# Kernel tuning notes

Hardware: AMD Instinct MI355X
Metric: run time of the kernel (lower is better)

Reference implementation:

```python
import jax, jax.numpy as jnp
import numpy as np

N_NODES = 100000
N_REL = 2
N_EDGES = 1600000  # per relation, avg degree 16
F_IN = 128
F_OUT = 64


def setup_inputs() -> dict:
    key = jax.random.key(0)
    k1, k2, k3, k4, k5 = jax.random.split(key, 5)
    x = jax.random.normal(k1, (N_NODES, F_IN), dtype=jnp.float32)
    src = jax.random.randint(k2, (N_REL, N_EDGES), 0, N_NODES)
    dst = jax.random.randint(k3, (N_REL, N_EDGES), 0, N_NODES)
    edge_w = jax.random.uniform(k4, (N_REL, N_EDGES), dtype=jnp.float32)
    # xavier_uniform with gain=1.414 as in the torch module
    limit = 1.414 * np.sqrt(6.0 / (F_IN + F_OUT))
    W = jax.random.uniform(k5, (F_IN, F_OUT), dtype=jnp.float32,
                           minval=-limit, maxval=limit)
    return {"x": x, "W": W, "edge_w": edge_w, "src": src, "dst": dst}


def reference(x, W, edge_w, src, dst):
    # Original: for each relation r, h = X @ W; support_r = A_r @ h; out = relu(sum_r support_r)
    # Since h is identical across relations and results are summed, compute
    # X @ W once and aggregate all relations' edges in one fused scatter-add.
    n = x.shape[0]
    h = x @ W  # [N, F_OUT]
    s = src.reshape(-1)  # [R*E]
    d = dst.reshape(-1)  # [R*E]
    w = edge_w.reshape(-1, 1)  # [R*E, 1]
    msgs = w * h[s]  # [R*E, F_OUT] weighted gather of source features
    agg = jax.ops.segment_sum(msgs, d, num_segments=n)  # [N, F_OUT]
    return jax.nn.relu(agg)
```

## Files before the change

### kernel.cpp

```cpp
#include <hip/hip_runtime.h>
#include <hip/hip_bf16.h>
#include <stdint.h>

#define F_IN 128
#define F_OUT 64
#define NPB 128
#define CHUNK 4096
#define NBUCK_MAX 1024
#define SRC_BITS 17
#define BCAP 5120

static __device__ __forceinline__ unsigned short f2bf(float f) {
    uint32_t u = __float_as_uint(f);
    u += 0x7FFF + ((u >> 16) & 1);
    return (unsigned short)(u >> 16);
}
static __device__ __forceinline__ float bf2f(unsigned short s) {
    return __uint_as_float((uint32_t)s << 16);
}

extern "C" __global__ __launch_bounds__(256) void k1_fused(
        const float* __restrict__ x, const float* __restrict__ W,
        unsigned short* __restrict__ h, int n,
        const int* __restrict__ src, const int* __restrict__ dst,
        const float* __restrict__ ew, int* __restrict__ cursor,
        uint32_t* __restrict__ rec32, uint8_t* __restrict__ dlo8,
        long nE, int nbuck, int partBlocks) {
    extern __shared__ char smem[];
    const int tid = threadIdx.x;

    if ((int)blockIdx.x < partBlocks) {
        uint32_t* srec  = (uint32_t*)smem;
        int*      cnt   = (int*)(smem + CHUNK * 4);
        int*      lbase = cnt + NBUCK_MAX;
        int*      gbase = lbase + NBUCK_MAX;
        int*      ssc   = gbase + NBUCK_MAX;
        uint8_t*  sdlo  = (uint8_t*)(ssc + 256);

        const int  c      = blockIdx.x;
        const long base   = (long)c * CHUNK;
        const long endl   = base + CHUNK < nE ? base + CHUNK : nE;
        const int  tcount = (int)(endl - base);

        for (int i = tid; i < NBUCK_MAX; i += 256) cnt[i] = 0;
        __syncthreads();
        for (int i = tid; i < tcount; i += 256)
            atomicAdd(&cnt[dst[base + i] >> 7], 1);
        __syncthreads();
        {
            const int t4 = tid * 4;
            const int a0 = cnt[t4], a1 = cnt[t4 + 1], a2 = cnt[t4 + 2], a3 = cnt[t4 + 3];
            const int ts = a0 + a1 + a2 + a3;
            ssc[tid] = ts; __syncthreads();
            for (int o = 1; o < 256; o <<= 1) {
                int t = (tid >= o) ? ssc[tid - o] : 0;
                __syncthreads();
                ssc[tid] += t;
                __syncthreads();
            }
            const int e = ssc[tid] - ts;
            lbase[t4]     = e;
            lbase[t4 + 1] = e + a0;
            lbase[t4 + 2] = e + a0 + a1;
            lbase[t4 + 3] = e + a0 + a1 + a2;
        }
        __syncthreads();
        for (int k = tid; k < nbuck; k += 256) {
            const int ck = cnt[k];
            if (ck) gbase[k] = k * BCAP + atomicAdd(&cursor[k], ck);
        }
        __syncthreads();
        for (int i = tid; i < NBUCK_MAX; i += 256) cnt[i] = lbase[i];
        __syncthreads();
        for (int i = tid; i < tcount; i += 256) {
            const int d = dst[base + i];
            const int k = d >> 7;
            const int pos = atomicAdd(&cnt[k], 1);
            uint32_t u = __float_as_uint(ew[base + i]);
            u += 0x10000u;
            srec[pos] = (u & 0xFFFE0000u) | (uint32_t)src[base + i];
            sdlo[pos] = (uint8_t)(d & (NPB - 1));
        }
        __syncthreads();
        for (int j = tid; j < tcount; j += 256) {
            int k = 0;
#pragma unroll
            for (int s = 512; s > 0; s >>= 1) {
                const int nk = k + s;
                if (nk < NBUCK_MAX && lbase[nk] <= j) k = nk;
            }
            const int gpos = gbase[k] + (j - lbase[k]);
            rec32[gpos] = srec[j];
            dlo8[gpos]  = sdlo[j];
        }
        return;
    }

    float* Ws = (float*)smem;
    float (*Xs)[F_IN + 4] = (float(*)[F_IN + 4])(smem + F_IN * F_OUT * 4);
    const int gb = (int)blockIdx.x - partBlocks;
    for (int i = tid; i < F_IN * F_OUT / 4; i += 256)
        ((float4*)Ws)[i] = ((const float4*)W)[i];
    const int row0 = gb * 16;
    for (int i = tid; i < 16 * 32; i += 256) {
        int r = i >> 5, cc = i & 31;
        if (row0 + r < n)
            *(float4*)&Xs[r][cc * 4] = *(const float4*)(x + (size_t)(row0 + r) * F_IN + cc * 4);
    }
    __syncthreads();
    const int cg = tid & 15;
    const int r  = tid >> 4;
    const int row = row0 + r;
    float4 acc = make_float4(0.f, 0.f, 0.f, 0.f);
#pragma unroll
    for (int k = 0; k < F_IN; ++k) {
        float  xv = Xs[r][k];
        float4 wv = ((const float4*)Ws)[k * 16 + cg];
        acc.x = fmaf(xv, wv.x, acc.x);
        acc.y = fmaf(xv, wv.y, acc.y);
        acc.z = fmaf(xv, wv.z, acc.z);
        acc.w = fmaf(xv, wv.w, acc.w);
    }
    if (row < n) {
        ushort4 o;
        o.x = f2bf(acc.x); o.y = f2bf(acc.y); o.z = f2bf(acc.z); o.w = f2bf(acc.w);
        *(ushort4*)(h + (size_t)row * F_OUT + cg * 4) = o;
    }
}

__global__ __launch_bounds__(256) void sortB(uint32_t* __restrict__ rec,
                                             const uint8_t* __restrict__ dlo8,
                                             const int* __restrict__ cursor,
                                             int* __restrict__ obeg,
                                             int* __restrict__ oend,
                                             int n, int nbuck) {
    __shared__ uint32_t ssort[BCAP];
    __shared__ int cnt[NPB], run[NPB], sa[NPB], sb[NPB];
    const int k   = blockIdx.x;
    const int tid = threadIdx.x;
    const int rbase = k * BCAP;
    int m = cursor[k];
    if (m > BCAP) m = BCAP;
    if (tid < NPB) cnt[tid] = 0;
    __syncthreads();
    for (int i = tid; i < m; i += 256)
        atomicAdd(&cnt[dlo8[(long)rbase + i]], 1);
    __syncthreads();
    if (tid < NPB) sa[tid] = cnt[tid];
    __syncthreads();
    int* pin = sa; int* pout = sb;
    for (int o = 1; o < NPB; o <<= 1) {
        if (tid < NPB) pout[tid] = pin[tid] + (tid >= o ? pin[tid - o] : 0);
        __syncthreads();
        int* t = pin; pin = pout; pout = t;
    }
    if (tid < NPB) {
        const int e = pin[tid] - cnt[tid];
        run[tid] = e;
        const int node = k * NPB + tid;
        if (node < n) {
            obeg[node] = rbase + e;
            oend[node] = rbase + e + cnt[tid];
        }
    }
    __syncthreads();
    for (int i = tid; i < m; i += 256) {
        const uint32_t r = rec[(long)rbase + i];
        const int d = dlo8[(long)rbase + i];
        ssort[atomicAdd(&run[d], 1)] = r;
    }
    __syncthreads();
    for (int i = tid; i < m; i += 256)
        rec[(long)rbase + i] = ssort[i];
}

__global__ __launch_bounds__(256, 8) void gather_nodes(
        const unsigned short* __restrict__ h,
        const uint32_t* __restrict__ rec,
        const int* __restrict__ obeg,
        const int* __restrict__ oend,
        float* __restrict__ out, int n) {
    const int wid  = threadIdx.x >> 6;
    const int lane = threadIdx.x & 63;
    const int node = blockIdx.x * 4 + wid;
    if (node >= n) return;
    int j = obeg[node];
    const int end = oend[node];
    const uint32_t M = (1u << SRC_BITS) - 1;
    float acc = 0.f;
    for (; j < end && (j & 3); ++j) {
        const uint32_t s = rec[j];
        acc = fmaf(__uint_as_float(s & 0xFFFE0000u),
                   bf2f(h[(int)((s & M) * 64u) + lane]), acc);
    }
    for (; j + 8 <= end; j += 8) {
        const uint4 A = *(const uint4*)(rec + j);
        const uint4 B = *(const uint4*)(rec + j + 4);
        const int i0 = (int)((A.x & M) * 64u) + lane;
        const int i1 = (int)((A.y & M) * 64u) + lane;
        const int i2 = (int)((A.z & M) * 64u) + lane;
        const int i3 = (int)((A.w & M) * 64u) + lane;
        const int i4 = (int)((B.x & M) * 64u) + lane;
        const int i5 = (int)((B.y & M) * 64u) + lane;
        const int i6 = (int)((B.z & M) * 64u) + lane;
        const int i7 = (int)((B.w & M) * 64u) + lane;
        const unsigned short d0 = h[i0];
        const unsigned short d1 = h[i1];
        const unsigned short d2 = h[i2];
        const unsigned short d3 = h[i3];
        const unsigned short d4 = h[i4];
        const unsigned short d5 = h[i5];
        const unsigned short d6 = h[i6];
        const unsigned short d7 = h[i7];
        acc = fmaf(__uint_as_float(A.x & 0xFFFE0000u), bf2f(d0), acc);
        acc = fmaf(__uint_as_float(A.y & 0xFFFE0000u), bf2f(d1), acc);
        acc = fmaf(__uint_as_float(A.z & 0xFFFE0000u), bf2f(d2), acc);
        acc = fmaf(__uint_as_float(A.w & 0xFFFE0000u), bf2f(d3), acc);
        acc = fmaf(__uint_as_float(B.x & 0xFFFE0000u), bf2f(d4), acc);
        acc = fmaf(__uint_as_float(B.y & 0xFFFE0000u), bf2f(d5), acc);
        acc = fmaf(__uint_as_float(B.z & 0xFFFE0000u), bf2f(d6), acc);
        acc = fmaf(__uint_as_float(B.w & 0xFFFE0000u), bf2f(d7), acc);
    }
    if (j + 4 <= end) {
        const uint4 A = *(const uint4*)(rec + j);
        const int i0 = (int)((A.x & M) * 64u) + lane;
        const int i1 = (int)((A.y & M) * 64u) + lane;
        const int i2 = (int)((A.z & M) * 64u) + lane;
        const int i3 = (int)((A.w & M) * 64u) + lane;
        const unsigned short d0 = h[i0];
        const unsigned short d1 = h[i1];
        const unsigned short d2 = h[i2];
        const unsigned short d3 = h[i3];
        acc = fmaf(__uint_as_float(A.x & 0xFFFE0000u), bf2f(d0), acc);
        acc = fmaf(__uint_as_float(A.y & 0xFFFE0000u), bf2f(d1), acc);
        acc = fmaf(__uint_as_float(A.z & 0xFFFE0000u), bf2f(d2), acc);
        acc = fmaf(__uint_as_float(A.w & 0xFFFE0000u), bf2f(d3), acc);
        j += 4;
    }
    for (; j < end; ++j) {
        const uint32_t s = rec[j];
        acc = fmaf(__uint_as_float(s & 0xFFFE0000u),
                   bf2f(h[(int)((s & M) * 64u) + lane]), acc);
    }
    out[(size_t)node * F_OUT + lane] = fmaxf(acc, 0.f);
}

__global__ __launch_bounds__(256) void gemm_only(const float* __restrict__ x,
                                                 const float* __restrict__ W,
                                                 unsigned short* __restrict__ h, int n) {
    __shared__ float Ws[F_IN * F_OUT];
    __shared__ float Xs[16][F_IN + 4];
    for (int i = threadIdx.x; i < F_IN * F_OUT / 4; i += 256)
        ((float4*)Ws)[i] = ((const float4*)W)[i];
    const int row0 = blockIdx.x * 16;
    for (int i = threadIdx.x; i < 16 * 32; i += 256) {
        int r = i >> 5, c = i & 31;
        if (row0 + r < n)
            *(float4*)&Xs[r][c * 4] = *(const float4*)(x + (size_t)(row0 + r) * F_IN + c * 4);
    }
    __syncthreads();
    const int cg = threadIdx.x & 15;
    const int r  = threadIdx.x >> 4;
    const int row = row0 + r;
    float4 acc = make_float4(0.f, 0.f, 0.f, 0.f);
#pragma unroll
    for (int k = 0; k < F_IN; ++k) {
        float  xv = Xs[r][k];
        float4 wv = ((const float4*)Ws)[k * 16 + cg];
        acc.x = fmaf(xv, wv.x, acc.x);
        acc.y = fmaf(xv, wv.y, acc.y);
        acc.z = fmaf(xv, wv.z, acc.z);
        acc.w = fmaf(xv, wv.w, acc.w);
    }
    if (row < n) {
        ushort4 o;
        o.x = f2bf(acc.x); o.y = f2bf(acc.y); o.z = f2bf(acc.z); o.w = f2bf(acc.w);
        *(ushort4*)(h + (size_t)row * F_OUT + cg * 4) = o;
    }
}

__global__ __launch_bounds__(256) void scatter_edges(const unsigned short* __restrict__ h,
                                                     const float* __restrict__ edge_w,
                                                     const int* __restrict__ src,
                                                     const int* __restrict__ dst,
                                                     float* __restrict__ out, long n_edges) {
    const int lane = threadIdx.x & 63;
    const long wave = ((long)blockIdx.x * blockDim.x + threadIdx.x) >> 6;
    const long nwaves = ((long)gridDim.x * blockDim.x) >> 6;
    for (long e = wave; e < n_edges; e += nwaves) {
        const float v = edge_w[e] * bf2f(h[(size_t)src[e] * F_OUT + lane]);
        atomicAdd(&out[(size_t)dst[e] * F_OUT + lane], v);
    }
}

__global__ __launch_bounds__(256) void relu_inplace(float* __restrict__ out, long n4) {
    long i = (long)blockIdx.x * blockDim.x + threadIdx.x;
    const long stride = (long)gridDim.x * blockDim.x;
    float4* p = (float4*)out;
    for (; i < n4; i += stride) {
        float4 v = p[i];
        v.x = v.x > 0.f ? v.x : 0.f;
        v.y = v.y > 0.f ? v.y : 0.f;
        v.z = v.z > 0.f ? v.z : 0.f;
        v.w = v.w > 0.f ? v.w : 0.f;
        p[i] = v;
    }
}

extern "C" void kernel_launch(void* const* d_in, const int* in_sizes, int n_in,
                              void* d_out, int out_size, void* d_ws, size_t ws_size,
                              hipStream_t stream) {
    const float* x      = (const float*)d_in[0];
    const float* W      = (const float*)d_in[1];
    const float* edge_w = (const float*)d_in[2];
    const int*   src    = (const int*)d_in[3];
    const int*   dst    = (const int*)d_in[4];
    float*       out    = (float*)d_out;

    const int  n_nodes = in_sizes[0] / F_IN;
    const long nE      = (long)in_sizes[2];
    const int  NBUCK   = (n_nodes + NPB - 1) / NPB;
    const int  NCHUNK  = (int)((nE + CHUNK - 1) / CHUNK);
    const int  gemmB   = (n_nodes + 15) / 16;

    size_t off = 0;
    auto seg = [&](size_t bytes) { size_t p = off; off = (off + bytes + 255) & ~(size_t)255; return p; };
    const size_t h_off    = seg((size_t)n_nodes * F_OUT * sizeof(unsigned short));
    const size_t rec_off  = seg((size_t)NBUCK * BCAP * sizeof(uint32_t));
    const size_t dlo_off  = seg((size_t)NBUCK * BCAP * sizeof(uint8_t));
    const size_t cur_off  = seg(NBUCK_MAX * sizeof(int));
    const size_t obeg_off = seg((size_t)n_nodes * sizeof(int));
    const size_t oend_off = seg((size_t)n_nodes * sizeof(int));
    char* ws = (char*)d_ws;

    unsigned short* h = (unsigned short*)(ws + h_off);

    if (off <= ws_size && NBUCK <= NBUCK_MAX && n_nodes <= (1 << SRC_BITS)) {
        uint32_t* rec    = (uint32_t*)(ws + rec_off);
        uint8_t*  dlo8   = (uint8_t*)(ws + dlo_off);
        int*      cursor = (int*)(ws + cur_off);
        int*      obeg   = (int*)(ws + obeg_off);
        int*      oend   = (int*)(ws + oend_off);

        hipMemsetAsync(cursor, 0, NBUCK_MAX * sizeof(int), stream);
        const size_t shmem = (size_t)(F_IN * F_OUT * 4 + 16 * (F_IN + 4) * 4);
        k1_fused<<<NCHUNK + gemmB, 256, shmem, stream>>>(x, W, h, n_nodes,
                                                         src, dst, edge_w, cursor,
                                                         rec, dlo8, nE, NBUCK, NCHUNK);
        sortB<<<NBUCK, 256, 0, stream>>>(rec, dlo8, cursor, obeg, oend, n_nodes, NBUCK);
        gather_nodes<<<(n_nodes + 3) / 4, 256, 0, stream>>>(h, rec, obeg, oend, out, n_nodes);
    } else {
        gemm_only<<<gemmB, 256, 0, stream>>>(x, W, h, n_nodes);
        hipMemsetAsync(d_out, 0, (size_t)out_size * sizeof(float), stream);
        scatter_edges<<<2048, 256, 0, stream>>>(h, edge_w, src, dst, out, nE);
        relu_inplace<<<1024, 256, 0, stream>>>(out, (long)out_size / 4);
    }
}
```

Measured before the change: 194.3 us.

## Split fused GEMM/partition kernel into separate launches with larger partition chunks

Replaces the single fused kernel, which ran the X@W GEMM blocks and the edge-bucketing blocks in one grid, with two kernels: a plain GEMM kernel and a dedicated partition kernel. The partition kernel now runs 512 threads per block over 8192-edge chunks. Each block keeps its own static shared memory instead of the larger dynamic allocation sized for the GEMM. This aims to raise occupancy and halve the per-chunk overhead and global cursor atomics, at the cost of an extra launch and losing the overlap between GEMM and partition work.

New measurement: 181.5 us. -6.6%, faster.

```diff
diff --git a/kernel.cpp b/kernel.cpp
--- a/kernel.cpp
+++ b/kernel.cpp
@@ -5,7 +5,7 @@
 #define F_IN 128
 #define F_OUT 64
 #define NPB 128
-#define CHUNK 4096
+#define CHUNK 8192
 #define NBUCK_MAX 1024
 #define SRC_BITS 17
 #define BCAP 5120
@@ -19,97 +19,22 @@
     return __uint_as_float((uint32_t)s << 16);
 }
 
-extern "C" __global__ __launch_bounds__(256) void k1_fused(
-        const float* __restrict__ x, const float* __restrict__ W,
-        unsigned short* __restrict__ h, int n,
-        const int* __restrict__ src, const int* __restrict__ dst,
-        const float* __restrict__ ew, int* __restrict__ cursor,
-        uint32_t* __restrict__ rec32, uint8_t* __restrict__ dlo8,
-        long nE, int nbuck, int partBlocks) {
-    extern __shared__ char smem[];
-    const int tid = threadIdx.x;
-
-    if ((int)blockIdx.x < partBlocks) {
-        uint32_t* srec  = (uint32_t*)smem;
-        int*      cnt   = (int*)(smem + CHUNK * 4);
-        int*      lbase = cnt + NBUCK_MAX;
-        int*      gbase = lbase + NBUCK_MAX;
-        int*      ssc   = gbase + NBUCK_MAX;
-        uint8_t*  sdlo  = (uint8_t*)(ssc + 256);
-
-        const int  c      = blockIdx.x;
-        const long base   = (long)c * CHUNK;
-        const long endl   = base + CHUNK < nE ? base + CHUNK : nE;
-        const int  tcount = (int)(endl - base);
-
-        for (int i = tid; i < NBUCK_MAX; i += 256) cnt[i] = 0;
-        __syncthreads();
-        for (int i = tid; i < tcount; i += 256)
-            atomicAdd(&cnt[dst[base + i] >> 7], 1);
-        __syncthreads();
-        {
-            const int t4 = tid * 4;
-            const int a0 = cnt[t4], a1 = cnt[t4 + 1], a2 = cnt[t4 + 2], a3 = cnt[t4 + 3];
-            const int ts = a0 + a1 + a2 + a3;
-            ssc[tid] = ts; __syncthreads();
-            for (int o = 1; o < 256; o <<= 1) {
-                int t = (tid >= o) ? ssc[tid - o] : 0;
-                __syncthreads();
-                ssc[tid] += t;
-                __syncthreads();
-            }
-            const int e = ssc[tid] - ts;
-            lbase[t4]     = e;
-            lbase[t4 + 1] = e + a0;
-            lbase[t4 + 2] = e + a0 + a1;
-            lbase[t4 + 3] = e + a0 + a1 + a2;
-        }
-        __syncthreads();
-        for (int k = tid; k < nbuck; k += 256) {
-            const int ck = cnt[k];
-            if (ck) gbase[k] = k * BCAP + atomicAdd(&cursor[k], ck);
-        }
-        __syncthreads();
-        for (int i = tid; i < NBUCK_MAX; i += 256) cnt[i] = lbase[i];
-        __syncthreads();
-        for (int i = tid; i < tcount; i += 256) {
-            const int d = dst[base + i];
-            const int k = d >> 7;
-            const int pos = atomicAdd(&cnt[k], 1);
-            uint32_t u = __float_as_uint(ew[base + i]);
-            u += 0x10000u;
-            srec[pos] = (u & 0xFFFE0000u) | (uint32_t)src[base + i];
-            sdlo[pos] = (uint8_t)(d & (NPB - 1));
-        }
-        __syncthreads();
-        for (int j = tid; j < tcount; j += 256) {
-            int k = 0;
-#pragma unroll
-            for (int s = 512; s > 0; s >>= 1) {
-                const int nk = k + s;
-                if (nk < NBUCK_MAX && lbase[nk] <= j) k = nk;
-            }
-            const int gpos = gbase[k] + (j - lbase[k]);
-            rec32[gpos] = srec[j];
-            dlo8[gpos]  = sdlo[j];
-        }
-        return;
-    }
-
-    float* Ws = (float*)smem;
-    float (*Xs)[F_IN + 4] = (float(*)[F_IN + 4])(smem + F_IN * F_OUT * 4);
-    const int gb = (int)blockIdx.x - partBlocks;
-    for (int i = tid; i < F_IN * F_OUT / 4; i += 256)
+__global__ __launch_bounds__(256) void gemm_xw(const float* __restrict__ x,
+                                               const float* __restrict__ W,
+                                               unsigned short* __restrict__ h, int n) {
+    __shared__ float Ws[F_IN * F_OUT];
+    __shared__ float Xs[16][F_IN + 4];
+    for (int i = threadIdx.x; i < F_IN * F_OUT / 4; i += 256)
         ((float4*)Ws)[i] = ((const float4*)W)[i];
-    const int row0 = gb * 16;
-    for (int i = tid; i < 16 * 32; i += 256) {
-        int r = i >> 5, cc = i & 31;
+    const int row0 = blockIdx.x * 16;
+    for (int i = threadIdx.x; i < 16 * 32; i += 256) {
+        int r = i >> 5, c = i & 31;
         if (row0 + r < n)
-            *(float4*)&Xs[r][cc * 4] = *(const float4*)(x + (size_t)(row0 + r) * F_IN + cc * 4);
-    }
-    __syncthreads();
-    const int cg = tid & 15;
-    const int r  = tid >> 4;
+            *(float4*)&Xs[r][c * 4] = *(const float4*)(x + (size_t)(row0 + r) * F_IN + c * 4);
+    }
+    __syncthreads();
+    const int cg = threadIdx.x & 15;
+    const int r  = threadIdx.x >> 4;
     const int row = row0 + r;
     float4 acc = make_float4(0.f, 0.f, 0.f, 0.f);
 #pragma unroll
@@ -125,6 +50,76 @@
         ushort4 o;
         o.x = f2bf(acc.x); o.y = f2bf(acc.y); o.z = f2bf(acc.z); o.w = f2bf(acc.w);
         *(ushort4*)(h + (size_t)row * F_OUT + cg * 4) = o;
+    }
+}
+
+__global__ __launch_bounds__(512) void partA(const int* __restrict__ src,
+                                             const int* __restrict__ dst,
+                                             const float* __restrict__ ew,
+                                             int* __restrict__ cursor,
+                                             uint32_t* __restrict__ rec32,
+                                             uint8_t* __restrict__ dlo8,
+                                             long nE, int nbuck) {
+    __shared__ uint32_t srec[CHUNK];
+    __shared__ uint8_t  sdlo[CHUNK];
+    __shared__ int cnt[NBUCK_MAX];
+    __shared__ int lbase[NBUCK_MAX];
+    __shared__ int gbase[NBUCK_MAX];
+    __shared__ int ssc[512];
+    const int c   = blockIdx.x;
+    const int tid = threadIdx.x;
+    const long base = (long)c * CHUNK;
+    const long endl = base + CHUNK < nE ? base + CHUNK : nE;
+    const int tcount = (int)(endl - base);
+
+    for (int i = tid; i < NBUCK_MAX; i += 512) cnt[i] = 0;
+    __syncthreads();
+    for (int i = tid; i < tcount; i += 512)
+        atomicAdd(&cnt[dst[base + i] >> 7], 1);
+    __syncthreads();
+    {
+        const int t2 = tid * 2;
+        const int a0 = cnt[t2], a1 = cnt[t2 + 1];
+        const int ts = a0 + a1;
+        ssc[tid] = ts; __syncthreads();
+        for (int o = 1; o < 512; o <<= 1) {
+            int t = (tid >= o) ? ssc[tid - o] : 0;
+            __syncthreads();
+            ssc[tid] += t;
+            __syncthreads();
+        }
+        const int excl = ssc[tid] - ts;
+        lbase[t2] = excl;
+        lbase[t2 + 1] = excl + a0;
+    }
+    __syncthreads();
+    for (int k = tid; k < nbuck; k += 512) {
+        const int ck = cnt[k];
+        if (ck) gbase[k] = k * BCAP + atomicAdd(&cursor[k], ck);
+    }
+    __syncthreads();
+    for (int i = tid; i < NBUCK_MAX; i += 512) cnt[i] = lbase[i];
+    __syncthreads();
+    for (int i = tid; i < tcount; i += 512) {
+        const int d = dst[base + i];
+        const int k = d >> 7;
+        const int pos = atomicAdd(&cnt[k], 1);
+        uint32_t u = __float_as_uint(ew[base + i]);
+        u += 0x10000u;
+        srec[pos] = (u & 0xFFFE0000u) | (uint32_t)src[base + i];
+        sdlo[pos] = (uint8_t)(d & (NPB - 1));
+    }
+    __syncthreads();
+    for (int j = tid; j < tcount; j += 512) {
+        int k = 0;
+#pragma unroll
+        for (int s = 512; s > 0; s >>= 1) {
+            const int nk = k + s;
+            if (nk < NBUCK_MAX && lbase[nk] <= j) k = nk;
+        }
+        const int gpos = gbase[k] + (j - lbase[k]);
+        rec32[gpos] = srec[j];
+        dlo8[gpos]  = sdlo[j];
     }
 }
 
@@ -245,40 +240,6 @@
     out[(size_t)node * F_OUT + lane] = fmaxf(acc, 0.f);
 }
 
-__global__ __launch_bounds__(256) void gemm_only(const float* __restrict__ x,
-                                                 const float* __restrict__ W,
-                                                 unsigned short* __restrict__ h, int n) {
-    __shared__ float Ws[F_IN * F_OUT];
-    __shared__ float Xs[16][F_IN + 4];
-    for (int i = threadIdx.x; i < F_IN * F_OUT / 4; i += 256)
-        ((float4*)Ws)[i] = ((const float4*)W)[i];
-    const int row0 = blockIdx.x * 16;
-    for (int i = threadIdx.x; i < 16 * 32; i += 256) {
-        int r = i >> 5, c = i & 31;
-        if (row0 + r < n)
-            *(float4*)&Xs[r][c * 4] = *(const float4*)(x + (size_t)(row0 + r) * F_IN + c * 4);
-    }
-    __syncthreads();
-    const int cg = threadIdx.x & 15;
-    const int r  = threadIdx.x >> 4;
-    const int row = row0 + r;
-    float4 acc = make_float4(0.f, 0.f, 0.f, 0.f);
-#pragma unroll
-    for (int k = 0; k < F_IN; ++k) {
-        float  xv = Xs[r][k];
-        float4 wv = ((const float4*)Ws)[k * 16 + cg];
-        acc.x = fmaf(xv, wv.x, acc.x);
-        acc.y = fmaf(xv, wv.y, acc.y);
-        acc.z = fmaf(xv, wv.z, acc.z);
-        acc.w = fmaf(xv, wv.w, acc.w);
-    }
-    if (row < n) {
-        ushort4 o;
-        o.x = f2bf(acc.x); o.y = f2bf(acc.y); o.z = f2bf(acc.z); o.w = f2bf(acc.w);
-        *(ushort4*)(h + (size_t)row * F_OUT + cg * 4) = o;
-    }
-}
-
 __global__ __launch_bounds__(256) void scatter_edges(const unsigned short* __restrict__ h,
                                                      const float* __restrict__ edge_w,
                                                      const int* __restrict__ src,
@@ -343,14 +304,12 @@
         int*      oend   = (int*)(ws + oend_off);
 
         hipMemsetAsync(cursor, 0, NBUCK_MAX * sizeof(int), stream);
-        const size_t shmem = (size_t)(F_IN * F_OUT * 4 + 16 * (F_IN + 4) * 4);
-        k1_fused<<<NCHUNK + gemmB, 256, shmem, stream>>>(x, W, h, n_nodes,
-                                                         src, dst, edge_w, cursor,
-                                                         rec, dlo8, nE, NBUCK, NCHUNK);
+        gemm_xw<<<gemmB, 256, 0, stream>>>(x, W, h, n_nodes);
+        partA<<<NCHUNK, 512, 0, stream>>>(src, dst, edge_w, cursor, rec, dlo8, nE, NBUCK);
         sortB<<<NBUCK, 256, 0, stream>>>(rec, dlo8, cursor, obeg, oend, n_nodes, NBUCK);
         gather_nodes<<<(n_nodes + 3) / 4, 256, 0, stream>>>(h, rec, obeg, oend, out, n_nodes);
     } else {
-        gemm_only<<<gemmB, 256, 0, stream>>>(x, W, h, n_nodes);
+        gemm_xw<<<gemmB, 256, 0, stream>>>(x, W, h, n_nodes);
         hipMemsetAsync(d_out, 0, (size_t)out_size * sizeof(float), stream);
         scatter_edges<<<2048, 256, 0, stream>>>(h, edge_w, src, dst, out, nE);
         relu_inplace<<<1024, 256, 0, stream>>>(out, (long)out_size / 4);
```
